# Kernel tuning notes

Hardware: AMD Instinct MI355X
Metric: run time of the kernel (lower is better)

## Reference

```python
import jax, jax.numpy as jnp
import numpy as np

B, S, E, H = 2, 2048, 1024, 16
D = E // H  # head_dim = 64
SCALE = 1.0 / np.sqrt(D)


def setup_inputs() -> dict:
    key = jax.random.key(0)
    ks = jax.random.split(key, 5)
    std = 0.02
    return {
        "x": jax.random.normal(ks[0], (B, S, E), dtype=jnp.float32),
        "wq": jax.random.normal(ks[1], (E, E), dtype=jnp.float32) * std,
        "wk": jax.random.normal(ks[2], (E, E), dtype=jnp.float32) * std,
        "wv": jax.random.normal(ks[3], (E, E), dtype=jnp.float32) * std,
        "wo": jax.random.normal(ks[4], (E, E), dtype=jnp.float32) * std,
    }


def reference(x, wq, wk, wv, wo):
    # Linear projections (torch Linear: y = x @ W.T); weights stored as [out, in]
    q = jnp.einsum('bse,fe->bsf', x, wq)
    k = jnp.einsum('bse,fe->bsf', x, wk)
    v = jnp.einsum('bse,fe->bsf', x, wv)
    # split heads -> [B, H, S, D]
    q = q.reshape(B, S, H, D).transpose(0, 2, 1, 3)
    k = k.reshape(B, S, H, D).transpose(0, 2, 1, 3)
    v = v.reshape(B, S, H, D).transpose(0, 2, 1, 3)
    # scaled dot-product scores [B, H, S, S]
    scores = jnp.einsum('bhqd,bhkd->bhqk', q, k) * SCALE
    # causal mask: -inf above diagonal
    causal = jnp.triu(jnp.full((S, S), -jnp.inf, dtype=scores.dtype), k=1)
    scores = scores + causal[None, None, :, :]
    attn = jax.nn.softmax(scores, axis=-1)
    # dropout p=0 -> identity
    out = jnp.einsum('bhqk,bhkd->bhqd', attn, v)
    out = out.transpose(0, 2, 1, 3).reshape(B, S, E)
    return jnp.einsum('bse,fe->bsf', out, wo)
```

## Files before the change

kernel.cpp:

```cpp
#include <hip/hip_runtime.h>
#include <hip/hip_bf16.h>

#define B_ 2
#define S_ 2048
#define E_ 1024
#define H_ 16
#define D_ 64
#define QKV_N 3072
#define C2_ 0.18033688011112042f

typedef __attribute__((ext_vector_type(8))) unsigned short ushort8_t;
typedef __attribute__((ext_vector_type(8))) short short8_t;
typedef __attribute__((ext_vector_type(4))) float f32x4;

__device__ __forceinline__ unsigned short f2b(float f) {
    union { float f; unsigned u; } x; x.f = f;
    unsigned r = x.u + 0x7FFFu + ((x.u >> 16) & 1u);
    return (unsigned short)(r >> 16);
}
__device__ __forceinline__ ushort2 pkbf(float a, float b) {
    union { __hip_bfloat162 h; ushort2 u; } c;
    c.h = __float22bfloat162_rn(make_float2(a, b));
    return c.u;
}
__device__ __forceinline__ void glds16(const unsigned short* g, unsigned short* l) {
    __builtin_amdgcn_global_load_lds((const __attribute__((address_space(1))) void*)g,
                                     (__attribute__((address_space(3))) void*)l, 16, 0, 0);
}

__global__ __launch_bounds__(256) void cast_all(const float* __restrict__ x,
                                                const float* __restrict__ wq,
                                                const float* __restrict__ wk,
                                                const float* __restrict__ wv,
                                                const float* __restrict__ wo,
                                                unsigned short* __restrict__ xb,
                                                unsigned short* __restrict__ wb) {
    int idx = blockIdx.x * 256 + threadIdx.x;
    const float* src; unsigned short* dst; float s = 1.f; int j;
    if (idx < 1048576) {
        src = x; dst = xb; j = idx;
    } else {
        j = idx - 1048576;
        int y = j >> 18;
        src = (y == 0) ? wq : (y == 1) ? wk : (y == 2) ? wv : wo;
        dst = wb + (size_t)y * 1048576;
        j &= 262143;
        if (y == 0) s = C2_;
    }
    float4 v = ((const float4*)src)[j];
    ushort2 lo = pkbf(v.x * s, v.y * s), hi = pkbf(v.z * s, v.w * s);
    ((ushort4*)dst)[j] = make_ushort4(lo.x, lo.y, hi.x, hi.y);
}

template <int TM, bool OUT_BF16, bool VT>
__device__ __forceinline__ void gemm_bt_body(const unsigned short* __restrict__ A,
                                             const unsigned short* __restrict__ Bt,
                                             void* __restrict__ Cout,
                                             int m0, int n0, int N, int K) {
    __shared__ unsigned short As[2 * TM * 32];
    __shared__ unsigned short Bs[2 * 128 * 32];
    const int tid = threadIdx.x;
    const int wave = tid >> 6;
    const int lane = tid & 63;
    const int wm = (wave >> 1) * (TM / 2);
    const int wn = (wave & 1) * 64;
    const int quad = lane >> 4;
    const int l15 = lane & 15;
    constexpr int MI = TM / 32;

    f32x4 acc[MI][4] = {};

    const int srow = lane >> 2;
    const int scb  = (lane & 3) * 8;
    const unsigned short* gB0 = Bt + (size_t)(n0 + wave * 32 + srow) * K + scb;
    const unsigned short* gB1 = gB0 + (size_t)16 * K;
    unsigned short* lB0 = Bs + wave * 1024;
    unsigned short* lB1 = lB0 + 512;
    const unsigned short* gA0;
    const unsigned short* gA1 = nullptr;
    unsigned short* lA0;
    unsigned short* lA1 = nullptr;
    if (TM == 128) {
        gA0 = A + (size_t)(m0 + wave * 32 + srow) * K + scb;
        gA1 = gA0 + (size_t)16 * K;
        lA0 = As + wave * 1024; lA1 = lA0 + 512;
    } else {
        gA0 = A + (size_t)(m0 + wave * 16 + srow) * K + scb;
        lA0 = As + wave * 512;
    }

    for (int k0 = 0; k0 < K; k0 += 64) {
        __syncthreads();
        glds16(gA0 + k0, lA0);
        glds16(gA0 + k0 + 32, lA0 + TM * 32);
        if (TM == 128) {
            glds16(gA1 + k0, lA1);
            glds16(gA1 + k0 + 32, lA1 + TM * 32);
        }
        glds16(gB0 + k0, lB0);
        glds16(gB0 + k0 + 32, lB0 + 128 * 32);
        glds16(gB1 + k0, lB1);
        glds16(gB1 + k0 + 32, lB1 + 128 * 32);
        __syncthreads();

#pragma unroll
        for (int h = 0; h < 2; ++h) {
            const unsigned short* ah = As + h * TM * 32;
            const unsigned short* bh = Bs + h * 128 * 32;
            short8_t af[MI], bfv[4];
#pragma unroll
            for (int mi = 0; mi < MI; ++mi)
                af[mi] = *(const short8_t*)(&ah[(wm + mi * 16 + l15) * 32 + quad * 8]);
#pragma unroll
            for (int ni = 0; ni < 4; ++ni)
                bfv[ni] = *(const short8_t*)(&bh[(wn + ni * 16 + l15) * 32 + quad * 8]);
#pragma unroll
            for (int mi = 0; mi < MI; ++mi)
#pragma unroll
                for (int ni = 0; ni < 4; ++ni)
                    acc[mi][ni] = __builtin_amdgcn_mfma_f32_16x16x32_bf16(
                        af[mi], bfv[ni], acc[mi][ni], 0, 0, 0);
        }
    }

    if (VT && n0 >= 2048) {
#pragma unroll
        for (int mi = 0; mi < MI; ++mi)
#pragma unroll
            for (int ni = 0; ni < 4; ++ni) {
                int col = n0 + wn + ni * 16 + l15;
                int r0  = m0 + wm + mi * 16 + quad * 4;
                int bb  = r0 >> 11, s = r0 & 2047;
                size_t drow = (size_t)bb * 2048 + 2 * (col - 2048) + (s >> 10);
                unsigned short* dp = (unsigned short*)Cout + drow * QKV_N + 2048 + (s & 1023);
                *(ushort4*)dp = make_ushort4(f2b(acc[mi][ni][0]), f2b(acc[mi][ni][1]),
                                             f2b(acc[mi][ni][2]), f2b(acc[mi][ni][3]));
            }
        return;
    }

#pragma unroll
    for (int mi = 0; mi < MI; ++mi)
#pragma unroll
        for (int ni = 0; ni < 4; ++ni)
#pragma unroll
            for (int r = 0; r < 4; ++r) {
                int row = m0 + wm + mi * 16 + quad * 4 + r;
                int col = n0 + wn + ni * 16 + l15;
                float val = acc[mi][ni][r];
                if (OUT_BF16)
                    ((unsigned short*)Cout)[(size_t)row * N + col] = f2b(val);
                else
                    ((float*)Cout)[(size_t)row * N + col] = val;
            }
}

__global__ __launch_bounds__(256, 3) void gemm_qkv(const unsigned short* __restrict__ xb,
                                                   const unsigned short* __restrict__ wqkv,
                                                   unsigned short* __restrict__ qkv) {
    int id = blockIdx.x + 24 * blockIdx.y;
    int sw = (id & 7) * 96 + (id >> 3);
    int n0 = (sw % 24) * 128;
    int m0 = (sw / 24) * 128;
    gemm_bt_body<128, true, true>(xb, wqkv, qkv, m0, n0, QKV_N, E_);
}

__global__ __launch_bounds__(256, 2) void gemm_out(const unsigned short* __restrict__ a,
                                                   const unsigned short* __restrict__ wob,
                                                   float* __restrict__ c) {
    int id = blockIdx.x + 8 * blockIdx.y;
    int sw = (id & 7) * 64 + (id >> 3);
    gemm_bt_body<64, false, false>(a, wob, c, (sw >> 3) * 64, (sw & 7) * 128, E_, E_);
}

__global__ __launch_bounds__(512, 4) void attn_kernel(const unsigned short* __restrict__ QKV,
                                                      unsigned short* __restrict__ O) {
    __shared__ unsigned short Ks[3][64 * 64];
    __shared__ unsigned short Vs[3][64 * 64];
    __shared__ unsigned short Ps[8][16 * 64];

    const int b = blockIdx.z, h = blockIdx.y;
    const int cx = blockIdx.x;
    const int c0 = (cx & 1) ? (15 - (cx >> 1)) : (cx >> 1);
    const int j = (b == 0) ? c0 : (15 - c0);
    const int tid = threadIdx.x;
    const int w = tid >> 6, lane = tid & 63;
    const int quad = lane >> 4, l15 = lane & 15;
    const int lx = l15 & 7;
    const int Q0 = j * 128 + w * 16;

    const size_t qo = (size_t)(b * S_ + Q0 + l15) * QKV_N + h * D_;
    short8_t bq0 = *(const short8_t*)(QKV + qo + quad * 8);
    short8_t bq1 = *(const short8_t*)(QKV + qo + 32 + quad * 8);

    f32x4 Oacc[4] = {};
    f32x4 Lacc = {};
    const int qg = Q0 + l15;
    short8_t ones;
#pragma unroll
    for (int i = 0; i < 8; ++i) ones[i] = (short)0x3F80;

    const int fo0 = ((quad) ^ lx) * 8;
    const int fo1 = ((4 + quad) ^ lx) * 8;
    const int krow = l15 * 64;
    int pwo[4];
#pragma unroll
    for (int tm = 0; tm < 4; ++tm)
        pwo[tm] = ((tm * 2 + (quad >> 1)) ^ lx) * 8 + (quad & 1) * 4;

    const int srow = tid >> 3;
    const int scb  = tid & 7;
    const int scw  = (scb ^ (srow & 7)) * 8;
    const int wofs = w * 512;
    const unsigned short* KsrcB = QKV + (size_t)(b * S_ + srow) * QKV_N + 1024 + h * D_ + scw;
    const unsigned short* VsrcB = QKV + (size_t)(b * S_ + 2 * (h * D_ + srow)) * QKV_N + 2048 + scw;

    auto issue = [&](int bn, int ktn) {
        glds16(KsrcB + (size_t)ktn * QKV_N, &Ks[bn][wofs]);
        glds16(VsrcB + (size_t)(ktn >> 10) * QKV_N + (ktn & 1023), &Vs[bn][wofs]);
    };

    const int ntiles = 2 * j + 2;
    issue(0, 0);
    issue(1, 64);
    int bi = 0;

    for (int t = 0; t < ntiles; ++t) {
        const int kt = t * 64;
        if (t + 1 < ntiles) asm volatile("s_waitcnt vmcnt(2)" ::: "memory");
        else                asm volatile("s_waitcnt vmcnt(0)" ::: "memory");
        __builtin_amdgcn_s_barrier();
        __builtin_amdgcn_sched_barrier(0);
        if (t + 2 < ntiles) {
            int b2 = bi + 2; if (b2 >= 3) b2 -= 3;
            issue(b2, kt + 128);
        }

        if (kt <= Q0 + 15) {
            const bool h2 = (kt + 32 <= Q0 + 15);

            if (kt + 63 <= Q0) {
#pragma unroll
                for (int tm = 0; tm < 4; ++tm) {
                    short8_t ak0 = *(const short8_t*)(&Ks[bi][tm * 1024 + krow + fo0]);
                    short8_t ak1 = *(const short8_t*)(&Ks[bi][tm * 1024 + krow + fo1]);
                    f32x4 st = {0.f, 0.f, 0.f, 0.f};
                    __builtin_amdgcn_s_setprio(1);
                    st = __builtin_amdgcn_mfma_f32_16x16x32_bf16(ak0, bq0, st, 0, 0, 0);
                    st = __builtin_amdgcn_mfma_f32_16x16x32_bf16(ak1, bq1, st, 0, 0, 0);
                    __builtin_amdgcn_s_setprio(0);
                    float p0 = __builtin_amdgcn_exp2f(st[0]);
                    float p1 = __builtin_amdgcn_exp2f(st[1]);
                    float p2 = __builtin_amdgcn_exp2f(st[2]);
                    float p3 = __builtin_amdgcn_exp2f(st[3]);
                    ushort2 a = pkbf(p0, p1), c2 = pkbf(p2, p3);
                    *(ushort4*)(&Ps[w][krow + pwo[tm]]) = make_ushort4(a.x, a.y, c2.x, c2.y);
                }
            } else {
                const int need = h2 ? 4 : 2;
                for (int tm = 0; tm < need; ++tm) {
                    if (kt + tm * 16 <= Q0 + 15) {
                        short8_t ak0 = *(const short8_t*)(&Ks[bi][tm * 1024 + krow + fo0]);
                        short8_t ak1 = *(const short8_t*)(&Ks[bi][tm * 1024 + krow + fo1]);
                        f32x4 st = {0.f, 0.f, 0.f, 0.f};
                        __builtin_amdgcn_s_setprio(1);
                        st = __builtin_amdgcn_mfma_f32_16x16x32_bf16(ak0, bq0, st, 0, 0, 0);
                        st = __builtin_amdgcn_mfma_f32_16x16x32_bf16(ak1, bq1, st, 0, 0, 0);
                        __builtin_amdgcn_s_setprio(0);
                        const int kvb = kt + tm * 16 + quad * 4;
                        float p0 = (kvb     > qg) ? 0.f : __builtin_amdgcn_exp2f(st[0]);
                        float p1 = (kvb + 1 > qg) ? 0.f : __builtin_amdgcn_exp2f(st[1]);
                        float p2 = (kvb + 2 > qg) ? 0.f : __builtin_amdgcn_exp2f(st[2]);
                        float p3 = (kvb + 3 > qg) ? 0.f : __builtin_amdgcn_exp2f(st[3]);
                        ushort2 a = pkbf(p0, p1), c2 = pkbf(p2, p3);
                        *(ushort4*)(&Ps[w][krow + pwo[tm]]) = make_ushort4(a.x, a.y, c2.x, c2.y);
                    } else {
                        *(ushort4*)(&Ps[w][krow + pwo[tm]]) = make_ushort4(0, 0, 0, 0);
                    }
                }
            }

#pragma unroll
            for (int kh = 0; kh < 2; ++kh) {
                if (kh == 1 && !h2) break;
                const int fo = kh ? fo1 : fo0;
                short8_t bv[4];
#pragma unroll
                for (int tn = 0; tn < 4; ++tn)
                    bv[tn] = *(const short8_t*)(&Vs[bi][tn * 1024 + krow + fo]);
                short8_t ap = *(const short8_t*)(&Ps[w][krow + fo]);
                __builtin_amdgcn_s_setprio(1);
#pragma unroll
                for (int tn = 0; tn < 4; ++tn)
                    Oacc[tn] = __builtin_amdgcn_mfma_f32_16x16x32_bf16(
                        ap, bv[tn], Oacc[tn], 0, 0, 0);
                Lacc = __builtin_amdgcn_mfma_f32_16x16x32_bf16(ap, ones, Lacc, 0, 0, 0);
                __builtin_amdgcn_s_setprio(0);
            }
        }

        bi = (bi + 1 == 3) ? 0 : bi + 1;
    }

    float lir[4];
#pragma unroll
    for (int r = 0; r < 4; ++r)
        lir[r] = 1.f / Lacc[r];
#pragma unroll
    for (int tn = 0; tn < 4; ++tn)
#pragma unroll
        for (int r = 0; r < 4; ++r) {
            int row = Q0 + quad * 4 + r;
            O[(size_t)(b * S_ + row) * E_ + h * D_ + tn * 16 + l15] =
                f2b(Oacc[tn][r] * lir[r]);
        }
}

extern "C" void kernel_launch(void* const* d_in, const int* in_sizes, int n_in,
                              void* d_out, int out_size, void* d_ws, size_t ws_size,
                              hipStream_t stream) {
    const float* x  = (const float*)d_in[0];
    const float* wq = (const float*)d_in[1];
    const float* wk = (const float*)d_in[2];
    const float* wv = (const float*)d_in[3];
    const float* wo = (const float*)d_in[4];
    float* out = (float*)d_out;

    unsigned short* ws   = (unsigned short*)d_ws;
    unsigned short* xb   = ws;
    unsigned short* wqkv = ws + 4194304;
    unsigned short* wob  = ws + 7340032;
    unsigned short* qkvb = ws + 8388608;
    unsigned short* ab   = ws + 20971520;

    cast_all<<<8192, 256, 0, stream>>>(x, wq, wk, wv, wo, xb, wqkv);
    gemm_qkv<<<dim3(24, 32), 256, 0, stream>>>(xb, wqkv, qkvb);
    attn_kernel<<<dim3(16, 16, 2), 512, 0, stream>>>(qkvb, ab);
    gemm_out<<<dim3(8, 64), 256, 0, stream>>>(ab, wob, out);
}
```

Baseline: 170.3 us.

## Process two 16-row query tiles per wave in attention to reuse K/V fragments

The attention block now uses 4 waves of 256 threads instead of 8, and each wave handles 32 query rows as two 16-row MFMA tiles sharing the same K and V LDS fragments. Each thread issues twice as many async global-to-LDS loads per tile, and the vmcnt wait is adjusted to match. The goal is to halve LDS reads of K/V per query row and reduce wave count overhead. The cost is doubled accumulator registers per wave and fewer waves available to hide latency.

```diff
diff --git a/kernel.cpp b/kernel.cpp
--- a/kernel.cpp
+++ b/kernel.cpp
@@ -173,11 +173,11 @@
     gemm_bt_body<64, false, false>(a, wob, c, (sw >> 3) * 64, (sw & 7) * 128, E_, E_);
 }
 
-__global__ __launch_bounds__(512, 4) void attn_kernel(const unsigned short* __restrict__ QKV,
+__global__ __launch_bounds__(256, 2) void attn_kernel(const unsigned short* __restrict__ QKV,
                                                       unsigned short* __restrict__ O) {
     __shared__ unsigned short Ks[3][64 * 64];
     __shared__ unsigned short Vs[3][64 * 64];
-    __shared__ unsigned short Ps[8][16 * 64];
+    __shared__ unsigned short Ps[4][2][16 * 64];
 
     const int b = blockIdx.z, h = blockIdx.y;
     const int cx = blockIdx.x;
@@ -187,15 +187,18 @@
     const int w = tid >> 6, lane = tid & 63;
     const int quad = lane >> 4, l15 = lane & 15;
     const int lx = l15 & 7;
-    const int Q0 = j * 128 + w * 16;
-
-    const size_t qo = (size_t)(b * S_ + Q0 + l15) * QKV_N + h * D_;
-    short8_t bq0 = *(const short8_t*)(QKV + qo + quad * 8);
-    short8_t bq1 = *(const short8_t*)(QKV + qo + 32 + quad * 8);
-
-    f32x4 Oacc[4] = {};
-    f32x4 Lacc = {};
-    const int qg = Q0 + l15;
+    const int Q0 = j * 128 + w * 32;
+
+    const size_t qoA = (size_t)(b * S_ + Q0 + l15) * QKV_N + h * D_;
+    const size_t qoB = qoA + (size_t)16 * QKV_N;
+    short8_t bqA0 = *(const short8_t*)(QKV + qoA + quad * 8);
+    short8_t bqA1 = *(const short8_t*)(QKV + qoA + 32 + quad * 8);
+    short8_t bqB0 = *(const short8_t*)(QKV + qoB + quad * 8);
+    short8_t bqB1 = *(const short8_t*)(QKV + qoB + 32 + quad * 8);
+
+    f32x4 OaccA[4] = {}, OaccB[4] = {};
+    f32x4 LaccA = {}, LaccB = {};
+    const int qgA = Q0 + l15, qgB = Q0 + 16 + l15;
     short8_t ones;
 #pragma unroll
     for (int i = 0; i < 8; ++i) ones[i] = (short)0x3F80;
@@ -212,12 +215,17 @@
     const int scb  = tid & 7;
     const int scw  = (scb ^ (srow & 7)) * 8;
     const int wofs = w * 512;
-    const unsigned short* KsrcB = QKV + (size_t)(b * S_ + srow) * QKV_N + 1024 + h * D_ + scw;
-    const unsigned short* VsrcB = QKV + (size_t)(b * S_ + 2 * (h * D_ + srow)) * QKV_N + 2048 + scw;
+    const unsigned short* KsrcB  = QKV + (size_t)(b * S_ + srow) * QKV_N + 1024 + h * D_ + scw;
+    const unsigned short* KsrcB2 = KsrcB + (size_t)32 * QKV_N;
+    const unsigned short* VsrcB  = QKV + (size_t)(b * S_ + 2 * (h * D_ + srow)) * QKV_N + 2048 + scw;
+    const unsigned short* VsrcB2 = VsrcB + (size_t)64 * QKV_N;
 
     auto issue = [&](int bn, int ktn) {
-        glds16(KsrcB + (size_t)ktn * QKV_N, &Ks[bn][wofs]);
-        glds16(VsrcB + (size_t)(ktn >> 10) * QKV_N + (ktn & 1023), &Vs[bn][wofs]);
+        size_t vo = (size_t)(ktn >> 10) * QKV_N + (ktn & 1023);
+        glds16(KsrcB  + (size_t)ktn * QKV_N, &Ks[bn][wofs]);
+        glds16(KsrcB2 + (size_t)ktn * QKV_N, &Ks[bn][wofs + 2048]);
+        glds16(VsrcB  + vo, &Vs[bn][wofs]);
+        glds16(VsrcB2 + vo, &Vs[bn][wofs + 2048]);
     };
 
     const int ntiles = 2 * j + 2;
@@ -227,7 +235,7 @@
 
     for (int t = 0; t < ntiles; ++t) {
         const int kt = t * 64;
-        if (t + 1 < ntiles) asm volatile("s_waitcnt vmcnt(2)" ::: "memory");
+        if (t + 1 < ntiles) asm volatile("s_waitcnt vmcnt(4)" ::: "memory");
         else                asm volatile("s_waitcnt vmcnt(0)" ::: "memory");
         __builtin_amdgcn_s_barrier();
         __builtin_amdgcn_sched_barrier(0);
@@ -236,46 +244,67 @@
             issue(b2, kt + 128);
         }
 
-        if (kt <= Q0 + 15) {
-            const bool h2 = (kt + 32 <= Q0 + 15);
+        if (kt <= Q0 + 31) {
+            const bool h2 = (kt + 32 <= Q0 + 31);
 
             if (kt + 63 <= Q0) {
 #pragma unroll
                 for (int tm = 0; tm < 4; ++tm) {
                     short8_t ak0 = *(const short8_t*)(&Ks[bi][tm * 1024 + krow + fo0]);
                     short8_t ak1 = *(const short8_t*)(&Ks[bi][tm * 1024 + krow + fo1]);
-                    f32x4 st = {0.f, 0.f, 0.f, 0.f};
+                    f32x4 stA = {0.f, 0.f, 0.f, 0.f}, stB = {0.f, 0.f, 0.f, 0.f};
                     __builtin_amdgcn_s_setprio(1);
-                    st = __builtin_amdgcn_mfma_f32_16x16x32_bf16(ak0, bq0, st, 0, 0, 0);
-                    st = __builtin_amdgcn_mfma_f32_16x16x32_bf16(ak1, bq1, st, 0, 0, 0);
+                    stA = __builtin_amdgcn_mfma_f32_16x16x32_bf16(ak0, bqA0, stA, 0, 0, 0);
+                    stA = __builtin_amdgcn_mfma_f32_16x16x32_bf16(ak1, bqA1, stA, 0, 0, 0);
+                    stB = __builtin_amdgcn_mfma_f32_16x16x32_bf16(ak0, bqB0, stB, 0, 0, 0);
+                    stB = __builtin_amdgcn_mfma_f32_16x16x32_bf16(ak1, bqB1, stB, 0, 0, 0);
                     __builtin_amdgcn_s_setprio(0);
-                    float p0 = __builtin_amdgcn_exp2f(st[0]);
-                    float p1 = __builtin_amdgcn_exp2f(st[1]);
-                    float p2 = __builtin_amdgcn_exp2f(st[2]);
-                    float p3 = __builtin_amdgcn_exp2f(st[3]);
-                    ushort2 a = pkbf(p0, p1), c2 = pkbf(p2, p3);
-                    *(ushort4*)(&Ps[w][krow + pwo[tm]]) = make_ushort4(a.x, a.y, c2.x, c2.y);
+                    float a0 = __builtin_amdgcn_exp2f(stA[0]);
+                    float a1 = __builtin_amdgcn_exp2f(stA[1]);
+                    float a2 = __builtin_amdgcn_exp2f(stA[2]);
+                    float a3 = __builtin_amdgcn_exp2f(stA[3]);
+                    float b0 = __builtin_amdgcn_exp2f(stB[0]);
+                    float b1 = __builtin_amdgcn_exp2f(stB[1]);
+                    float b2f = __builtin_amdgcn_exp2f(stB[2]);
+                    float b3 = __builtin_amdgcn_exp2f(stB[3]);
+                    ushort2 pa = pkbf(a0, a1), pc = pkbf(a2, a3);
+                    ushort2 qa = pkbf(b0, b1), qc = pkbf(b2f, b3);
+                    *(ushort4*)(&Ps[w][0][krow + pwo[tm]]) = make_ushort4(pa.x, pa.y, pc.x, pc.y);
+                    *(ushort4*)(&Ps[w][1][krow + pwo[tm]]) = make_ushort4(qa.x, qa.y, qc.x, qc.y);
                 }
             } else {
                 const int need = h2 ? 4 : 2;
                 for (int tm = 0; tm < need; ++tm) {
-                    if (kt + tm * 16 <= Q0 + 15) {
-                        short8_t ak0 = *(const short8_t*)(&Ks[bi][tm * 1024 + krow + fo0]);
-                        short8_t ak1 = *(const short8_t*)(&Ks[bi][tm * 1024 + krow + fo1]);
+                    short8_t ak0 = *(const short8_t*)(&Ks[bi][tm * 1024 + krow + fo0]);
+                    short8_t ak1 = *(const short8_t*)(&Ks[bi][tm * 1024 + krow + fo1]);
+                    const int kvb = kt + tm * 16 + quad * 4;
+                    {
                         f32x4 st = {0.f, 0.f, 0.f, 0.f};
                         __builtin_amdgcn_s_setprio(1);
-                        st = __builtin_amdgcn_mfma_f32_16x16x32_bf16(ak0, bq0, st, 0, 0, 0);
-                        st = __builtin_amdgcn_mfma_f32_16x16x32_bf16(ak1, bq1, st, 0, 0, 0);
+                        st = __builtin_amdgcn_mfma_f32_16x16x32_bf16(ak0, bqB0, st, 0, 0, 0);
+                        st = __builtin_amdgcn_mfma_f32_16x16x32_bf16(ak1, bqB1, st, 0, 0, 0);
                         __builtin_amdgcn_s_setprio(0);
-                        const int kvb = kt + tm * 16 + quad * 4;
-                        float p0 = (kvb     > qg) ? 0.f : __builtin_amdgcn_exp2f(st[0]);
-                        float p1 = (kvb + 1 > qg) ? 0.f : __builtin_amdgcn_exp2f(st[1]);
-                        float p2 = (kvb + 2 > qg) ? 0.f : __builtin_amdgcn_exp2f(st[2]);
-                        float p3 = (kvb + 3 > qg) ? 0.f : __builtin_amdgcn_exp2f(st[3]);
+                        float p0 = (kvb     > qgB) ? 0.f : __builtin_amdgcn_exp2f(st[0]);
+                        float p1 = (kvb + 1 > qgB) ? 0.f : __builtin_amdgcn_exp2f(st[1]);
+                        float p2 = (kvb + 2 > qgB) ? 0.f : __builtin_amdgcn_exp2f(st[2]);
+                        float p3 = (kvb + 3 > qgB) ? 0.f : __builtin_amdgcn_exp2f(st[3]);
                         ushort2 a = pkbf(p0, p1), c2 = pkbf(p2, p3);
-                        *(ushort4*)(&Ps[w][krow + pwo[tm]]) = make_ushort4(a.x, a.y, c2.x, c2.y);
+                        *(ushort4*)(&Ps[w][1][krow + pwo[tm]]) = make_ushort4(a.x, a.y, c2.x, c2.y);
+                    }
+                    if (kt + tm * 16 <= Q0 + 15) {
+                        f32x4 st = {0.f, 0.f, 0.f, 0.f};
+                        __builtin_amdgcn_s_setprio(1);
+                        st = __builtin_amdgcn_mfma_f32_16x16x32_bf16(ak0, bqA0, st, 0, 0, 0);
+                        st = __builtin_amdgcn_mfma_f32_16x16x32_bf16(ak1, bqA1, st, 0, 0, 0);
+                        __builtin_amdgcn_s_setprio(0);
+                        float p0 = (kvb     > qgA) ? 0.f : __builtin_amdgcn_exp2f(st[0]);
+                        float p1 = (kvb + 1 > qgA) ? 0.f : __builtin_amdgcn_exp2f(st[1]);
+                        float p2 = (kvb + 2 > qgA) ? 0.f : __builtin_amdgcn_exp2f(st[2]);
+                        float p3 = (kvb + 3 > qgA) ? 0.f : __builtin_amdgcn_exp2f(st[3]);
+                        ushort2 a = pkbf(p0, p1), c2 = pkbf(p2, p3);
+                        *(ushort4*)(&Ps[w][0][krow + pwo[tm]]) = make_ushort4(a.x, a.y, c2.x, c2.y);
                     } else {
-                        *(ushort4*)(&Ps[w][krow + pwo[tm]]) = make_ushort4(0, 0, 0, 0);
+                        *(ushort4*)(&Ps[w][0][krow + pwo[tm]]) = make_ushort4(0, 0, 0, 0);
                     }
                 }
             }
@@ -288,13 +317,19 @@
 #pragma unroll
                 for (int tn = 0; tn < 4; ++tn)
                     bv[tn] = *(const short8_t*)(&Vs[bi][tn * 1024 + krow + fo]);
-                short8_t ap = *(const short8_t*)(&Ps[w][krow + fo]);
+                short8_t apA = *(const short8_t*)(&Ps[w][0][krow + fo]);
+                short8_t apB = *(const short8_t*)(&Ps[w][1][krow + fo]);
                 __builtin_amdgcn_s_setprio(1);
 #pragma unroll
                 for (int tn = 0; tn < 4; ++tn)
-                    Oacc[tn] = __builtin_amdgcn_mfma_f32_16x16x32_bf16(
-                        ap, bv[tn], Oacc[tn], 0, 0, 0);
-                Lacc = __builtin_amdgcn_mfma_f32_16x16x32_bf16(ap, ones, Lacc, 0, 0, 0);
+                    OaccA[tn] = __builtin_amdgcn_mfma_f32_16x16x32_bf16(
+                        apA, bv[tn], OaccA[tn], 0, 0, 0);
+                LaccA = __builtin_amdgcn_mfma_f32_16x16x32_bf16(apA, ones, LaccA, 0, 0, 0);
+#pragma unroll
+                for (int tn = 0; tn < 4; ++tn)
+                    OaccB[tn] = __builtin_amdgcn_mfma_f32_16x16x32_bf16(
+                        apB, bv[tn], OaccB[tn], 0, 0, 0);
+                LaccB = __builtin_amdgcn_mfma_f32_16x16x32_bf16(apB, ones, LaccB, 0, 0, 0);
                 __builtin_amdgcn_s_setprio(0);
             }
         }
@@ -302,17 +337,22 @@
         bi = (bi + 1 == 3) ? 0 : bi + 1;
     }
 
-    float lir[4];
-#pragma unroll
-    for (int r = 0; r < 4; ++r)
-        lir[r] = 1.f / Lacc[r];
+    float lirA[4], lirB[4];
+#pragma unroll
+    for (int r = 0; r < 4; ++r) {
+        lirA[r] = 1.f / LaccA[r];
+        lirB[r] = 1.f / LaccB[r];
+    }
 #pragma unroll
     for (int tn = 0; tn < 4; ++tn)
 #pragma unroll
         for (int r = 0; r < 4; ++r) {
-            int row = Q0 + quad * 4 + r;
-            O[(size_t)(b * S_ + row) * E_ + h * D_ + tn * 16 + l15] =
-                f2b(Oacc[tn][r] * lir[r]);
+            int rowA = Q0 + quad * 4 + r;
+            O[(size_t)(b * S_ + rowA) * E_ + h * D_ + tn * 16 + l15] =
+                f2b(OaccA[tn][r] * lirA[r]);
+            int rowB = Q0 + 16 + quad * 4 + r;
+            O[(size_t)(b * S_ + rowB) * E_ + h * D_ + tn * 16 + l15] =
+                f2b(OaccB[tn][r] * lirB[r]);
         }
 }
 
@@ -335,6 +375,6 @@
 
     cast_all<<<8192, 256, 0, stream>>>(x, wq, wk, wv, wo, xb, wqkv);
     gemm_qkv<<<dim3(24, 32), 256, 0, stream>>>(xb, wqkv, qkvb);
-    attn_kernel<<<dim3(16, 16, 2), 512, 0, stream>>>(qkvb, ab);
+    attn_kernel<<<dim3(16, 16, 2), 256, 0, stream>>>(qkvb, ab);
     gemm_out<<<dim3(8, 64), 256, 0, stream>>>(ab, wob, out);
 }
```

Result: slower. 173.9 us (+2.1%).
